# Kernel optimization log

Hardware: AMD Instinct MI355X
Metric: run time of the kernel (lower is better)

The kernel has to match this reference:

```python
import jax, jax.numpy as jnp
import numpy as np

# Cleaned/faithful JAX port of TATLMPLayer. The original torch code has obvious
# typos (edge_type_feature_embedding used before assignment, self.weight_mlp vs
# self._weight_mlp, missing dim= in concatenate, elementwise mult of (B,E,K) with
# (K,D)); we implement the clearly intended math: two-level masked-softmax
# message passing over an incidence matrix H, gumbel-softmax typed edge
# embeddings, and a 4-head cross-attention to polyline features.

NEG_SLOPE = 0.01  # torch leaky_relu default
TAU = 0.5         # gumbel-softmax temperature 1/2


def _mlp(x, W1, b1, W2, b2):
    return jnp.maximum(x @ W1 + b1, 0.0) @ W2 + b2


def setup_inputs() -> dict:
    B, N, E, P, D, T, K, Hd = 2, 256, 512, 256, 128, 8, 8, 256
    key = jax.random.key(0)
    ks = jax.random.split(key, 40)
    g = lambda i, shape, s=0.05: jax.random.normal(ks[i], shape, dtype=jnp.float32) * s
    return {
        "agent_features": jax.random.normal(ks[0], (B, N, D), dtype=jnp.float32),
        "agent_types": jax.random.uniform(ks[1], (B, N, T), dtype=jnp.float32),
        "polyline_features": jax.random.normal(ks[2], (B, P, D), dtype=jnp.float32),
        "H": (jax.random.uniform(ks[3], (B, E, N)) < 0.1).astype(jnp.float32),
        "type_emb": g(4, (K, D)),
        "w_W1": g(5, (2 * D, Hd)), "w_b1": g(6, (Hd,)), "w_W2": g(7, (Hd, 1)), "w_b2": g(8, (1,)),
        "d_W1": g(9, (D + T, Hd)), "d_b1": g(10, (Hd,)), "d_W2": g(11, (Hd, K)), "d_b2": g(12, (K,)),
        "f_W1": g(13, (D + T, Hd)), "f_b1": g(14, (Hd,)), "f_W2": g(15, (Hd, 1)), "f_b2": g(16, (1,)),
        "o_W1": g(17, (4 * D, Hd)), "o_b1": g(18, (Hd,)), "o_W2": g(19, (Hd, D)), "o_b2": g(20, (D,)),
        "q_W": g(21, (3 * D, D)), "q_b": g(22, (D,)),
        "k_W": g(23, (D, D)), "k_b": g(24, (D,)),
        "v_W": g(25, (D, D)), "v_b": g(26, (D,)),
        "iq_W": g(27, (D, D)), "iq_b": g(28, (D,)),
        "ik_W": g(29, (D, D)), "ik_b": g(30, (D,)),
        "iv_W": g(31, (D, D)), "iv_b": g(32, (D,)),
        "op_W": g(33, (D, D)), "op_b": g(34, (D,)),
    }


def reference(agent_features, agent_types, polyline_features, H, type_emb,
              w_W1, w_b1, w_W2, w_b2, d_W1, d_b1, d_W2, d_b2,
              f_W1, f_b1, f_W2, f_b2, o_W1, o_b1, o_W2, o_b2,
              q_W, q_b, k_W, k_b, v_W, v_b,
              iq_W, iq_b, ik_W, ik_b, iv_W, iv_b, op_W, op_b):
    B, N, D = agent_features.shape
    E = H.shape[1]

    # level 1: incidence-aggregated edge features
    ef_init = jnp.einsum('ben,bnd->bed', H, agent_features)            # (B,E,D)
    pair = jnp.concatenate([
        jnp.broadcast_to(ef_init[:, :, None, :], (B, E, N, D)),
        jnp.broadcast_to(agent_features[:, None, :, :], (B, E, N, D))], axis=-1)
    ew = _mlp(pair, w_W1, w_b1, w_W2, w_b2)[..., 0]                    # (B,E,N)
    Hw = jax.nn.softmax(ew * H, axis=2) * H
    edge_features = jnp.einsum('ben,bnd->bed', Hw, agent_features)     # (B,E,D)

    # typed edge embedding via gumbel-softmax over edge types
    edge_type = jnp.einsum('ben,bnt->bet', H, agent_types)             # (B,E,T)
    et = jnp.concatenate([edge_features, edge_type], axis=-1)          # (B,E,D+T)
    logits = _mlp(et, d_W1, d_b1, d_W2, d_b2)                          # (B,E,K)
    u = jax.random.uniform(jax.random.key(42), logits.shape, minval=1e-6, maxval=1.0 - 1e-6)
    gumbel = -jnp.log(-jnp.log(u))
    distribution = jax.nn.softmax((logits + gumbel) / TAU, axis=-1)
    factor = jax.nn.sigmoid(_mlp(et, f_W1, f_b1, f_W2, f_b2))          # (B,E,1)
    edge_type_embedding = jnp.einsum('bek,kd->bed', factor * distribution, type_emb)

    # level 2: masked edge->agent message passing
    pair2 = jnp.concatenate([
        jnp.broadcast_to(edge_type_embedding[:, :, None, :], (B, E, N, D)),
        jnp.broadcast_to(agent_features[:, None, :, :], (B, E, N, D))], axis=-1)
    pair2 = pair2 * H[..., None]
    hw2 = jnp.where(_mlp(pair2, w_W1, w_b1, w_W2, w_b2)[..., 0] > 0,
                    _mlp(pair2, w_W1, w_b1, w_W2, w_b2)[..., 0], 0.0)
    # leaky relu (single-eval form)
    raw2 = _mlp(pair2, w_W1, w_b1, w_W2, w_b2)[..., 0]
    hw2 = jnp.where(raw2 > 0, raw2, NEG_SLOPE * raw2)                  # (B,E,N)
    Hw2 = jax.nn.softmax(hw2, axis=2) * H
    msg = jnp.einsum('ben,bef->bnf', Hw2,
                     jnp.concatenate([edge_features, edge_type_embedding], axis=-1))
    agent_feat = jnp.concatenate([msg, agent_features], axis=-1)       # (B,N,3D)

    # cross-attention to polylines (4 heads)
    Q = agent_feat @ q_W + q_b
    Kp = polyline_features @ k_W + k_b
    Vp = polyline_features @ v_W + v_b
    q2 = Q @ iq_W + iq_b
    k2 = Kp @ ik_W + ik_b
    v2 = Vp @ iv_W + iv_b
    nh, hd = 4, D // 4
    qh = q2.reshape(B, N, nh, hd)
    kh = k2.reshape(B, -1, nh, hd)
    vh = v2.reshape(B, -1, nh, hd)
    att = jax.nn.softmax(jnp.einsum('bqhd,bkhd->bhqk', qh, kh) / jnp.sqrt(jnp.float32(hd)), axis=-1)
    o = jnp.einsum('bhqk,bkhd->bqhd', att, vh).reshape(B, N, D)
    polyline_new = o @ op_W + op_b                                     # (B,N,D)

    agent_new = _mlp(jnp.concatenate([agent_feat, polyline_new], axis=-1),
                     o_W1, o_b1, o_W2, o_b2)                           # (B,N,D)
    return agent_new, polyline_new
```

## Files before the change

### kernel.cpp

```cpp
#include <hip/hip_runtime.h>
#include <math.h>

#define BB 2
#define NN 256
#define EE 512
#define PP 256
#define DD 128
#define TT 8
#define KK 8
#define HDIM 256

#define WS_G      0
#define WS_C0     8192
#define WS_EF0    8256
#define WS_ETYPE  139328
#define WS_V      147520
#define WS_EDGEF  278592
#define WS_ETE    409664
#define WS_HWT    540736
#define WS_AGF    802880
#define WS_Q2     999488
#define WS_K2     1065024
#define WS_V2     1130560

__device__ inline unsigned rotl32(unsigned x, int d){ return (x<<d)|(x>>(32-d)); }

__device__ inline float bits_to_gumbel(unsigned bits){
  float f = __uint_as_float((bits>>9)|0x3f800000u) - 1.0f;
  const float minv = 1e-6f;
  const float maxv = 1.0f - 1e-6f;
  float u = f*(maxv-minv) + minv;
  u = fmaxf(minv, u);
  return -logf(-logf(u));
}

__device__ __forceinline__ void f4fma(float4& a, float x, const float4& w){
  a.x += x*w.x; a.y += x*w.y; a.z += x*w.z; a.w += x*w.w;
}

__device__ __forceinline__ void block_reduce4_max(float v[4], float* wred){
  int lane = threadIdx.x & 63, wid = threadIdx.x >> 6;
  #pragma unroll
  for (int s=32;s>0;s>>=1){
    #pragma unroll
    for (int r=0;r<4;r++){ float o = __shfl_xor(v[r], s, 64); v[r] = fmaxf(v[r],o); }
  }
  if (lane==0){
    #pragma unroll
    for (int r=0;r<4;r++) wred[wid*4+r]=v[r];
  }
  __syncthreads();
  #pragma unroll
  for (int r=0;r<4;r++)
    v[r] = fmaxf(fmaxf(wred[0*4+r],wred[1*4+r]), fmaxf(wred[2*4+r],wred[3*4+r]));
  __syncthreads();
}

__device__ __forceinline__ void block_reduce4_sum(float v[4], float* wred){
  int lane = threadIdx.x & 63, wid = threadIdx.x >> 6;
  #pragma unroll
  for (int s=32;s>0;s>>=1){
    #pragma unroll
    for (int r=0;r<4;r++){ v[r] += __shfl_xor(v[r], s, 64); }
  }
  if (lane==0){
    #pragma unroll
    for (int r=0;r<4;r++) wred[wid*4+r]=v[r];
  }
  __syncthreads();
  #pragma unroll
  for (int r=0;r<4;r++)
    v[r] = (wred[0*4+r]+wred[1*4+r]) + (wred[2*4+r]+wred[3*4+r]);
  __syncthreads();
}

__global__ void prep_kernel(float* g, float* c0, const float* w_b1,
                            const float* w_W2, const float* w_b2,
                            const float* Hm, const float* af, const float* at,
                            float* ef0, float* etype,
                            const float* wW1, float* Vout){
  __shared__ int   ecomp[NN];
  __shared__ int   wcnt[4];
  __shared__ float accl[2][DD];
  __shared__ float acctl[2][TT];
  __shared__ float xs[4][DD];
  __shared__ float part[4*4*HDIM];
  __shared__ float wred[16];
  int blk = blockIdx.x;
  int t = threadIdx.x;
  int lane = t & 63, wid = t >> 6;

  if (blk < 16){
    int j = blk*256 + t;
    {
      const unsigned k0=0u, k1=42u;
      const unsigned ks2 = k0^k1^0x1BD11BDAu;
      unsigned x0 = (unsigned)j, x1 = (unsigned)j + 4096u;
      const int r0[4]={13,15,26,6}, r1[4]={17,29,16,24};
      x0 += k0; x1 += k1;
      #pragma unroll
      for(int i=0;i<4;i++){ x0+=x1; x1=rotl32(x1,r0[i]); x1^=x0; }
      x0+=k1; x1+=ks2+1u;
      #pragma unroll
      for(int i=0;i<4;i++){ x0+=x1; x1=rotl32(x1,r1[i]); x1^=x0; }
      x0+=ks2; x1+=k0+2u;
      #pragma unroll
      for(int i=0;i<4;i++){ x0+=x1; x1=rotl32(x1,r0[i]); x1^=x0; }
      x0+=k0; x1+=k1+3u;
      #pragma unroll
      for(int i=0;i<4;i++){ x0+=x1; x1=rotl32(x1,r1[i]); x1^=x0; }
      x0+=k1; x1+=ks2+4u;
      #pragma unroll
      for(int i=0;i<4;i++){ x0+=x1; x1=rotl32(x1,r0[i]); x1^=x0; }
      x0+=ks2; x1+=k0+5u;
      g[j]      = bits_to_gumbel(x0);
      g[j+4096] = bits_to_gumbel(x1);
    }
    if (blk == 0){
      float v4[4];
      v4[0] = fmaxf(w_b1[t],0.f)*w_W2[t]; v4[1]=0.f; v4[2]=0.f; v4[3]=0.f;
      block_reduce4_sum(v4, wred);
      if (t==0) c0[0] = v4[0] + w_b2[0];
    }
  } else if (blk < 16+BB*EE){
    int be = blk - 16;
    int b  = be / EE;
    const float* Hrow = Hm + (size_t)be*NN;
    int n = t;
    bool pred = (Hrow[n] != 0.f);
    unsigned long long mask = __ballot(pred);
    if (lane==0) wcnt[wid] = __popcll(mask);
    int off = __popcll(mask & ((1ull<<lane)-1ull));
    __syncthreads();
    int wb = 0;
    for (int ww=0; ww<wid; ww++) wb += wcnt[ww];
    if (pred) ecomp[wb+off] = n;
    int total = wcnt[0]+wcnt[1]+wcnt[2]+wcnt[3];
    __syncthreads();
    int d = t & 127, h2 = t >> 7;
    float acc = 0.f, acct = 0.f;
    for (int i=h2; i<total; i+=2){
      int n2 = ecomp[i];
      acc += af[((size_t)b*NN+n2)*DD + d];
      if (d < TT) acct += at[((size_t)b*NN+n2)*TT + d];
    }
    accl[h2][d] = acc;
    if (d < TT) acctl[h2][d] = acct;
    __syncthreads();
    if (t < DD) ef0[(size_t)be*DD + t] = accl[0][t] + accl[1][t];
    if (t < TT) etype[(size_t)be*TT + t] = acctl[0][t] + acctl[1][t];
  } else {
    int r0 = (blk - (16+BB*EE))*4;
    const float* W = wW1 + (size_t)DD*HDIM;
    for (int i=t;i<4*DD;i+=256) xs[i>>7][i&127] = af[(size_t)(r0+(i>>7))*DD + (i&127)];
    __syncthreads();
    int c = (t&63)*4, ks = t>>6;
    float4 acc[4];
    #pragma unroll
    for (int r=0;r<4;r++) acc[r]=make_float4(0.f,0.f,0.f,0.f);
    #pragma unroll 8
    for (int i=ks*32; i<ks*32+32; i++){
      float4 w = *(const float4*)&W[(size_t)i*HDIM + c];
      #pragma unroll
      for (int r=0;r<4;r++) f4fma(acc[r], xs[r][i], w);
    }
    #pragma unroll
    for (int r=0;r<4;r++) *(float4*)&part[(ks*4+r)*HDIM + c] = acc[r];
    __syncthreads();
    #pragma unroll
    for (int r=0;r<4;r++){
      float s = (part[(0*4+r)*HDIM+t] + part[(1*4+r)*HDIM+t])
              + (part[(2*4+r)*HDIM+t] + part[(3*4+r)*HDIM+t]);
      Vout[(size_t)(r0+r)*HDIM + t] = s;
    }
  }
}

__global__ void l1_fused_kernel(const float* ef0, const float* Vm, const float* Hm,
                                const float* af, const float* wW1, const float* wb1,
                                const float* wW2, const float* wb2, float* edgef){
  __shared__ float xs[4][DD];
  __shared__ float part[4*4*HDIM];
  __shared__ float u[4][HDIM];
  __shared__ float w2l[HDIM];
  __shared__ float hwls[4][NN];
  __shared__ float wred[16];
  __shared__ int   ncomp[4][NN];
  __shared__ float ncw[4][NN];
  __shared__ int   ncnt[4];
  int e0 = blockIdx.x*4;
  int b  = e0 >> 9;
  int t  = threadIdx.x;
  int lane = t & 63, wid = t >> 6;

  for (int i=t;i<4*DD;i+=256) xs[i>>7][i&127] = ef0[(size_t)(e0+(i>>7))*DD + (i&127)];
  w2l[t] = wW2[t];
  __syncthreads();
  {
    int c = (t&63)*4, ks = t>>6;
    float4 acc[4];
    #pragma unroll
    for (int r=0;r<4;r++) acc[r]=make_float4(0.f,0.f,0.f,0.f);
    #pragma unroll 8
    for (int i=ks*32; i<ks*32+32; i++){
      float4 w = *(const float4*)&wW1[(size_t)i*HDIM + c];
      #pragma unroll
      for (int r=0;r<4;r++) f4fma(acc[r], xs[r][i], w);
    }
    #pragma unroll
    for (int r=0;r<4;r++) *(float4*)&part[(ks*4+r)*HDIM + c] = acc[r];
  }
  __syncthreads();
  {
    float bv = wb1[t];
    #pragma unroll
    for (int r=0;r<4;r++){
      float s = (part[(0*4+r)*HDIM+t] + part[(1*4+r)*HDIM+t])
              + (part[(2*4+r)*HDIM+t] + part[(3*4+r)*HDIM+t]);
      u[r][t] = s + bv;
    }
  }
  __syncthreads();
  int n = t;
  const float4* Vrow = (const float4*)(Vm + ((size_t)(b*NN)+n)*HDIM);
  float acc[4]={0.f,0.f,0.f,0.f};
  #pragma unroll 4
  for (int ii=0;ii<HDIM/4;ii++){
    float4 v = Vrow[ii];
    float w0=w2l[4*ii+0], w1=w2l[4*ii+1], wc=w2l[4*ii+2], w3=w2l[4*ii+3];
    #pragma unroll
    for (int r=0;r<4;r++){
      acc[r] += fmaxf(u[r][4*ii+0]+v.x,0.f)*w0
              + fmaxf(u[r][4*ii+1]+v.y,0.f)*w1
              + fmaxf(u[r][4*ii+2]+v.z,0.f)*wc
              + fmaxf(u[r][4*ii+3]+v.w,0.f)*w3;
    }
  }
  float b2v = wb2[0];
  float x[4], hv[4];
  #pragma unroll
  for (int r=0;r<4;r++){
    hv[r] = Hm[(size_t)(e0+r)*NN + n];
    x[r] = (hv[r]!=0.f) ? (acc[r]+b2v) : 0.f;
  }
  float m4[4]={x[0],x[1],x[2],x[3]};
  block_reduce4_max(m4, wred);
  float p4[4];
  #pragma unroll
  for (int r=0;r<4;r++) p4[r]=expf(x[r]-m4[r]);
  float s4[4]={p4[0],p4[1],p4[2],p4[3]};
  block_reduce4_sum(s4, wred);
  #pragma unroll
  for (int r=0;r<4;r++)
    hwls[r][n] = (hv[r]!=0.f) ? p4[r]/s4[r] : 0.f;
  __syncthreads();
  {
    int r = wid;
    int base = 0;
    #pragma unroll
    for (int c4=0;c4<4;c4++){
      int n2 = c4*64 + lane;
      float w = hwls[r][n2];
      bool pred = (w != 0.f);
      unsigned long long mask = __ballot(pred);
      int off = __popcll(mask & ((1ull<<lane)-1ull));
      if (pred){ ncomp[r][base+off] = n2; ncw[r][base+off] = w; }
      base += __popcll(mask);
    }
    if (lane==0) ncnt[r] = base;
  }
  __syncthreads();
  {
    int d = t & 127, eh = t >> 7;
    #pragma unroll
    for (int rr=0;rr<2;rr++){
      int r = eh*2 + rr;
      int tot = ncnt[r];
      float a = 0.f;
      for (int i=0;i<tot;i++)
        a += ncw[r][i]*af[((size_t)b*NN+ncomp[r][i])*DD + d];
      edgef[(size_t)(e0+r)*DD + d] = a;
    }
  }
}

__global__ void l2_fused_kernel(const float* edgef, const float* etype, const float* g,
                                const float* dW1, const float* db1, const float* dW2, const float* db2,
                                const float* fW1, const float* fb1, const float* fW2, const float* fb2,
                                const float* type_emb,
                                const float* wW1, const float* wb1, const float* wW2, const float* wb2,
                                const float* c0p, const float* Hm, const float* Vm,
                                float* ete_g, float* HwT){
  __shared__ float et4[4][DD+TT+8];
  __shared__ float part[4*4*HDIM];
  __shared__ float hd4[4][HDIM];
  __shared__ float w2s[HDIM*KK];
  __shared__ float redsm[256];
  __shared__ float wred[16];
  __shared__ float facs[4];
  __shared__ float zz[4][KK];
  __shared__ float pzs[4][KK];
  __shared__ float fdv[4][KK];
  int e0 = blockIdx.x*4;
  int b  = e0 >> 9;
  int t  = threadIdx.x;
  const int KW = DD+TT;

  for (int i=t;i<4*KW;i+=256){
    int r=i/KW, cc=i%KW;
    et4[r][cc] = (cc<DD) ? edgef[(size_t)(e0+r)*DD+cc] : etype[(size_t)(e0+r)*TT + (cc-DD)];
  }
  for (int i=t;i<HDIM*KK;i+=256) w2s[i] = dW2[i];
  __syncthreads();
  int c=(t&63)*4, ks=t>>6;
  {
    float4 a[4];
    #pragma unroll
    for (int r=0;r<4;r++) a[r]=make_float4(0.f,0.f,0.f,0.f);
    #pragma unroll 4
    for (int i=ks*34;i<ks*34+34;i++){
      float4 w = *(const float4*)&dW1[(size_t)i*HDIM+c];
      #pragma unroll
      for (int r=0;r<4;r++) f4fma(a[r], et4[r][i], w);
    }
    #pragma unroll
    for (int r=0;r<4;r++) *(float4*)&part[(ks*4+r)*HDIM+c]=a[r];
  }
  __syncthreads();
  {
    float bd = db1[t];
    #pragma unroll
    for (int r=0;r<4;r++){
      float s = (part[(0*4+r)*HDIM+t]+part[(1*4+r)*HDIM+t])
              + (part[(2*4+r)*HDIM+t]+part[(3*4+r)*HDIM+t]);
      hd4[r][t] = fmaxf(s+bd, 0.f);
    }
  }
  __syncthreads();
  {
    float4 a[4];
    #pragma unroll
    for (int r=0;r<4;r++) a[r]=make_float4(0.f,0.f,0.f,0.f);
    #pragma unroll 4
    for (int i=ks*34;i<ks*34+34;i++){
      float4 w = *(const float4*)&fW1[(size_t)i*HDIM+c];
      #pragma unroll
      for (int r=0;r<4;r++) f4fma(a[r], et4[r][i], w);
    }
    #pragma unroll
    for (int r=0;r<4;r++) *(float4*)&part[(ks*4+r)*HDIM+c]=a[r];
  }
  __syncthreads();
  {
    float bf = fb1[t], fw = fW2[t];
    float v4[4];
    #pragma unroll
    for (int r=0;r<4;r++){
      float s = (part[(0*4+r)*HDIM+t]+part[(1*4+r)*HDIM+t])
              + (part[(2*4+r)*HDIM+t]+part[(3*4+r)*HDIM+t]);
      v4[r] = fmaxf(s+bf,0.f)*fw;
    }
    block_reduce4_sum(v4, wred);
    if (t<4) facs[t] = 1.f/(1.f+expf(-(v4[t]+fb2[0])));
  }
  {
    int rr_ = t>>6, kk_ = (t>>3)&7, jj_ = t&7;
    float lp = 0.f;
    #pragma unroll 4
    for (int h=jj_*32; h<jj_*32+32; h++) lp += hd4[rr_][h]*w2s[h*KK + kk_];
    redsm[t] = lp;
  }
  __syncthreads();
  if (t < 32){
    int r = t>>3, k = t&7;
    float s = db2[k] + g[(size_t)(e0+r)*KK + k];
    #pragma unroll
    for (int j=0;j<8;j++) s += redsm[(r<<6)|(k<<3)|j];
    zz[r][k] = s*2.0f;
  }
  __syncthreads();
  if (t < 32){
    int r = t>>3, k = t&7;
    float m = zz[r][0];
    #pragma unroll
    for (int k2=1;k2<KK;k2++) m = fmaxf(m, zz[r][k2]);
    pzs[r][k] = expf(zz[r][k]-m);
  }
  __syncthreads();
  if (t < 32){
    int r = t>>3, k = t&7;
    float s = 0.f;
    #pragma unroll
    for (int k2=0;k2<KK;k2++) s += pzs[r][k2];
    fdv[r][k] = facs[r]*pzs[r][k]/s;
  }
  __syncthreads();
  {
    int d = t&127;
    #pragma unroll
    for (int rr=0;rr<2;rr++){
      int r = 2*rr + (t>>7);
      float a = 0.f;
      #pragma unroll
      for (int k=0;k<KK;k++) a += fdv[r][k]*type_emb[(size_t)k*DD + d];
      et4[r][d] = a;
      ete_g[(size_t)(e0+r)*DD + d] = a;
    }
    w2s[t] = wW2[t];
  }
  __syncthreads();
  {
    float4 a[4];
    #pragma unroll
    for (int r=0;r<4;r++) a[r]=make_float4(0.f,0.f,0.f,0.f);
    #pragma unroll 8
    for (int i=ks*32;i<ks*32+32;i++){
      float4 w = *(const float4*)&wW1[(size_t)i*HDIM+c];
      #pragma unroll
      for (int r=0;r<4;r++) f4fma(a[r], et4[r][i], w);
    }
    #pragma unroll
    for (int r=0;r<4;r++) *(float4*)&part[(ks*4+r)*HDIM+c]=a[r];
  }
  __syncthreads();
  {
    float bv = wb1[t];
    #pragma unroll
    for (int r=0;r<4;r++){
      float s = (part[(0*4+r)*HDIM+t]+part[(1*4+r)*HDIM+t])
              + (part[(2*4+r)*HDIM+t]+part[(3*4+r)*HDIM+t]);
      hd4[r][t] = s + bv;
    }
  }
  __syncthreads();
  {
    int n = t;
    const float4* Vrow = (const float4*)(Vm + ((size_t)(b*NN)+n)*HDIM);
    float acc[4]={0.f,0.f,0.f,0.f};
    #pragma unroll 4
    for (int ii=0;ii<HDIM/4;ii++){
      float4 v = Vrow[ii];
      float w0=w2s[4*ii+0], w1=w2s[4*ii+1], wc=w2s[4*ii+2], w3=w2s[4*ii+3];
      #pragma unroll
      for (int r=0;r<4;r++){
        acc[r] += fmaxf(hd4[r][4*ii+0]+v.x,0.f)*w0
                + fmaxf(hd4[r][4*ii+1]+v.y,0.f)*w1
                + fmaxf(hd4[r][4*ii+2]+v.z,0.f)*wc
                + fmaxf(hd4[r][4*ii+3]+v.w,0.f)*w3;
      }
    }
    float b2v = wb2[0];
    float c0 = c0p[0];
    float x[4], hv[4];
    #pragma unroll
    for (int r=0;r<4;r++){
      hv[r] = Hm[(size_t)(e0+r)*NN + n];
      float raw = (hv[r]!=0.f) ? (acc[r]+b2v) : c0;
      x[r] = raw>0.f ? raw : 0.01f*raw;
    }
    float m4[4]={x[0],x[1],x[2],x[3]};
    block_reduce4_max(m4, wred);
    float p4[4];
    #pragma unroll
    for (int r=0;r<4;r++) p4[r]=expf(x[r]-m4[r]);
    float s4[4]={p4[0],p4[1],p4[2],p4[3]};
    block_reduce4_sum(s4, wred);
    int eb = e0 & 511;
    float4 o4;
    o4.x = (hv[0]!=0.f)? p4[0]/s4[0] : 0.f;
    o4.y = (hv[1]!=0.f)? p4[1]/s4[1] : 0.f;
    o4.z = (hv[2]!=0.f)? p4[2]/s4[2] : 0.f;
    o4.w = (hv[3]!=0.f)? p4[3]/s4[3] : 0.f;
    *(float4*)(HwT + ((size_t)(b*NN)+n)*EE + eb) = o4;
  }
}

__global__ void msg_kernel(const float* HwT, const float* edgef, const float* ete,
                           const float* af, float* agf){
  __shared__ int   ecomp[EE];
  __shared__ float wcomp[EE];
  __shared__ int wcnt[4];
  int bn = blockIdx.x; int b = bn>>8; int f = threadIdx.x;
  int lane = f & 63, wid = f >> 6;
  const float* wrow = HwT + (size_t)bn*EE;
  int total = 0;
  #pragma unroll
  for (int p=0;p<2;p++){
    int e = p*256 + f;
    float w = wrow[e];
    bool pred = (w != 0.f);
    unsigned long long mask = __ballot(pred);
    if (lane==0) wcnt[wid] = __popcll(mask);
    int off = __popcll(mask & ((1ull<<lane)-1ull));
    __syncthreads();
    int wb = total;
    for (int ww=0; ww<wid; ww++) wb += wcnt[ww];
    if (pred){ ecomp[wb+off] = e; wcomp[wb+off] = w; }
    total += wcnt[0]+wcnt[1]+wcnt[2]+wcnt[3];
    __syncthreads();
  }
  float acc = 0.f;
  const float* srcbase = (f < DD) ? (edgef + (size_t)b*EE*DD + f)
                                  : (ete   + (size_t)b*EE*DD + (f-DD));
  for (int i=0;i<total;i++){
    acc += wcomp[i] * srcbase[(size_t)ecomp[i]*DD];
  }
  agf[(size_t)bn*(3*DD)+f] = acc;
  if (f < DD) agf[(size_t)bn*(3*DD) + 2*DD + f] = af[(size_t)bn*DD + f];
}

__device__ __forceinline__ void mlp128_lds(const float (*in)[DD], const float* W, const float* bias,
                                           float (*outl)[DD], float* part, int t){
  int c=(t&31)*4, ks=t>>5;
  float4 a[4];
  #pragma unroll
  for (int r=0;r<4;r++) a[r]=make_float4(0.f,0.f,0.f,0.f);
  #pragma unroll 4
  for (int i=ks*16;i<ks*16+16;i++){
    float4 w = *(const float4*)&W[(size_t)i*DD+c];
    #pragma unroll
    for (int r=0;r<4;r++) f4fma(a[r], in[r][i], w);
  }
  #pragma unroll
  for (int r=0;r<4;r++) *(float4*)&part[(ks*4+r)*DD+c]=a[r];
  __syncthreads();
  int cc=t&127, rh=t>>7;
  for (int rr=rh; rr<4; rr+=2){
    float s=0.f;
    #pragma unroll
    for (int k2=0;k2<8;k2++) s+=part[(k2*4+rr)*DD+cc];
    outl[rr][cc]=s+bias[cc];
  }
  __syncthreads();
}

__device__ __forceinline__ void mlp128_glob(const float (*in)[DD], const float* W, const float* bias,
                                            float* dst, int r0, float* part, int t){
  int c=(t&31)*4, ks=t>>5;
  float4 a[4];
  #pragma unroll
  for (int r=0;r<4;r++) a[r]=make_float4(0.f,0.f,0.f,0.f);
  #pragma unroll 4
  for (int i=ks*16;i<ks*16+16;i++){
    float4 w = *(const float4*)&W[(size_t)i*DD+c];
    #pragma unroll
    for (int r=0;r<4;r++) f4fma(a[r], in[r][i], w);
  }
  #pragma unroll
  for (int r=0;r<4;r++) *(float4*)&part[(ks*4+r)*DD+c]=a[r];
  __syncthreads();
  int cc=t&127, rh=t>>7;
  for (int rr=rh; rr<4; rr+=2){
    float s=0.f;
    #pragma unroll
    for (int k2=0;k2<8;k2++) s+=part[(k2*4+rr)*DD+cc];
    dst[(size_t)(r0+rr)*DD+cc]=s+bias[cc];
  }
  __syncthreads();
}

__global__ void q2kv_kernel(const float* agf, const float* qW, const float* qb,
                            const float* iqW, const float* iqb,
                            const float* pf,
                            const float* kW, const float* kb, const float* ikW, const float* ikb,
                            const float* vW, const float* vb, const float* ivW, const float* ivb,
                            float* q2, float* k2, float* v2){
  __shared__ float xs[4][3*DD];
  __shared__ float bufA[4][DD];
  __shared__ float bufB[4][DD];
  __shared__ float part[8*4*DD];
  int t = threadIdx.x;
  if (blockIdx.x < 128){
    int r0 = blockIdx.x*4;
    #pragma unroll
    for (int r=0;r<4;r++)
      for (int cc=t;cc<3*DD;cc+=256) xs[r][cc] = agf[(size_t)(r0+r)*(3*DD)+cc];
    __syncthreads();
    int c=(t&31)*4, ks=t>>5;
    float4 a[4];
    #pragma unroll
    for (int r=0;r<4;r++) a[r]=make_float4(0.f,0.f,0.f,0.f);
    #pragma unroll 4
    for (int i=ks*48;i<ks*48+48;i++){
      float4 w = *(const float4*)&qW[(size_t)i*DD+c];
      #pragma unroll
      for (int r=0;r<4;r++) f4fma(a[r], xs[r][i], w);
    }
    #pragma unroll
    for (int r=0;r<4;r++) *(float4*)&part[(ks*4+r)*DD+c]=a[r];
    __syncthreads();
    int cc=t&127, rh=t>>7;
    for (int rr=rh; rr<4; rr+=2){
      float s=0.f;
      #pragma unroll
      for (int k2_=0;k2_<8;k2_++) s+=part[(k2_*4+rr)*DD+cc];
      bufA[rr][cc]=s+qb[cc];
    }
    __syncthreads();
    mlp128_glob(bufA, iqW, iqb, q2, r0, part, t);
  } else {
    int r0 = (blockIdx.x-128)*4;
    for (int i=t;i<4*DD;i+=256) bufA[i>>7][i&127] = pf[(size_t)(r0+(i>>7))*DD + (i&127)];
    __syncthreads();
    mlp128_lds (bufA, kW, kb, bufB, part, t);
    mlp128_glob(bufB, ikW, ikb, k2, r0, part, t);
    mlp128_lds (bufA, vW, vb, bufB, part, t);
    mlp128_glob(bufB, ivW, ivb, v2, r0, part, t);
  }
}

__global__ void attn2_kernel(const float* q2, const float* k2, const float* v2,
                             const float* op_W, const float* op_b, float* pnew){
  __shared__ float qr[2][DD];
  __shared__ float att[2][4][PP+1];
  __shared__ float o_l[2][DD];
  __shared__ float part[8*2*DD];
  int r0 = blockIdx.x*2; int b = r0 >> 8; int t = threadIdx.x;
  for (int i=t;i<2*DD;i+=256) qr[i>>7][i&127] = q2[(size_t)(r0+(i>>7))*DD + (i&127)];
  __syncthreads();
  const float scale = 0.17677669529663687f;
  const float* krow = k2 + ((size_t)(b*PP) + t)*DD;
  #pragma unroll
  for (int h=0;h<4;h++){
    const float4* k4 = (const float4*)(krow + h*32);
    float s[2]={0.f,0.f};
    #pragma unroll
    for (int jj=0;jj<8;jj++){
      float4 kk = k4[jj];
      #pragma unroll
      for (int r=0;r<2;r++){
        s[r] += qr[r][h*32+jj*4+0]*kk.x + qr[r][h*32+jj*4+1]*kk.y
              + qr[r][h*32+jj*4+2]*kk.z + qr[r][h*32+jj*4+3]*kk.w;
      }
    }
    #pragma unroll
    for (int r=0;r<2;r++) att[r][h][t] = s[r]*scale;
  }
  __syncthreads();
  {
    int lane = t & 63, wid = t >> 6;
    for (int q = wid; q < 8; q += 4){
      int r = q >> 2, h = q & 3;
      float v0 = att[r][h][lane],     v1 = att[r][h][lane+64],
            ve = att[r][h][lane+128], v3 = att[r][h][lane+192];
      float m = fmaxf(fmaxf(v0,v1), fmaxf(ve,v3));
      #pragma unroll
      for (int s2=32;s2>0;s2>>=1) m = fmaxf(m, __shfl_xor(m, s2, 64));
      float e0 = expf(v0-m), e1 = expf(v1-m), e2 = expf(ve-m), e3 = expf(v3-m);
      float ss = (e0+e1)+(e2+e3);
      #pragma unroll
      for (int s2=32;s2>0;s2>>=1) ss += __shfl_xor(ss, s2, 64);
      float inv = 1.f/ss;
      att[r][h][lane] = e0*inv; att[r][h][lane+64] = e1*inv;
      att[r][h][lane+128] = e2*inv; att[r][h][lane+192] = e3*inv;
    }
  }
  __syncthreads();
  int c=(t&31)*4, ps=t>>5; int h2 = c>>5;
  {
    float4 acc[2];
    #pragma unroll
    for (int r=0;r<2;r++) acc[r]=make_float4(0.f,0.f,0.f,0.f);
    #pragma unroll 4
    for (int i=0;i<32;i++){
      int p = ps*32+i;
      float4 v = *(const float4*)&v2[((size_t)(b*PP)+p)*DD + c];
      #pragma unroll
      for (int r=0;r<2;r++) f4fma(acc[r], att[r][h2][p], v);
    }
    #pragma unroll
    for (int r=0;r<2;r++) *(float4*)&part[(ps*2+r)*DD+c]=acc[r];
  }
  __syncthreads();
  {
    int cc=t&127, r=t>>7;
    float s=0.f;
    #pragma unroll
    for (int k2_=0;k2_<8;k2_++) s+=part[(k2_*2+r)*DD+cc];
    o_l[r][cc]=s;
  }
  __syncthreads();
  {
    float4 a2[2];
    #pragma unroll
    for (int r=0;r<2;r++) a2[r]=make_float4(0.f,0.f,0.f,0.f);
    #pragma unroll 4
    for (int i=ps*16;i<ps*16+16;i++){
      float4 w = *(const float4*)&op_W[(size_t)i*DD + c];
      #pragma unroll
      for (int r=0;r<2;r++) f4fma(a2[r], o_l[r][i], w);
    }
    #pragma unroll
    for (int r=0;r<2;r++) *(float4*)&part[(ps*2+r)*DD+c]=a2[r];
  }
  __syncthreads();
  {
    int cc=t&127, r=t>>7;
    float s=0.f;
    #pragma unroll
    for (int k2_=0;k2_<8;k2_++) s+=part[(k2_*2+r)*DD+cc];
    pnew[(size_t)(r0+r)*DD+cc]=s+op_b[cc];
  }
}

__global__ void final2_kernel(const float* agf, const float* pnewv,
                              const float* oW1, const float* ob1,
                              const float* oW2, const float* ob2, float* anew){
  __shared__ float xs[2][4*DD];
  __shared__ float hid[2][HDIM];
  __shared__ float part[4*2*HDIM];
  int r0 = blockIdx.x*2; int t = threadIdx.x;
  for (int i=t;i<2*(4*DD);i+=256){
    int r = i>>9, cc = i&511;
    xs[r][cc] = (cc<3*DD) ? agf[(size_t)(r0+r)*(3*DD)+cc]
                          : pnewv[(size_t)(r0+r)*DD + (cc-3*DD)];
  }
  __syncthreads();
  {
    int c=(t&63)*4, ks=t>>6;
    float4 acc[2];
    #pragma unroll
    for (int r=0;r<2;r++) acc[r]=make_float4(0.f,0.f,0.f,0.f);
    #pragma unroll 8
    for (int i=ks*128;i<ks*128+128;i++){
      float4 w = *(const float4*)&oW1[(size_t)i*HDIM+c];
      #pragma unroll
      for (int r=0;r<2;r++) f4fma(acc[r], xs[r][i], w);
    }
    #pragma unroll
    for (int r=0;r<2;r++) *(float4*)&part[(ks*2+r)*HDIM+c]=acc[r];
  }
  __syncthreads();
  {
    float bv = ob1[t];
    #pragma unroll
    for (int r=0;r<2;r++){
      float s = (part[(0*2+r)*HDIM+t]+part[(1*2+r)*HDIM+t])
              + (part[(2*2+r)*HDIM+t]+part[(3*2+r)*HDIM+t]);
      hid[r][t] = fmaxf(s+bv, 0.f);
    }
  }
  __syncthreads();
  {
    int c2=(t&31)*4, ks2=t>>5;
    float4 a2[2];
    #pragma unroll
    for (int r=0;r<2;r++) a2[r]=make_float4(0.f,0.f,0.f,0.f);
    #pragma unroll 8
    for (int h=ks2*32;h<ks2*32+32;h++){
      float4 w = *(const float4*)&oW2[(size_t)h*DD+c2];
      #pragma unroll
      for (int r=0;r<2;r++) f4fma(a2[r], hid[r][h], w);
    }
    #pragma unroll
    for (int r=0;r<2;r++) *(float4*)&part[(ks2*2+r)*DD+c2]=a2[r];
  }
  __syncthreads();
  {
    int cc=t&127, r=t>>7;
    float s=0.f;
    #pragma unroll
    for (int k2_=0;k2_<8;k2_++) s+=part[(k2_*2+r)*DD+cc];
    anew[(size_t)(r0+r)*DD+cc]=s+ob2[cc];
  }
}

extern "C" void kernel_launch(void* const* d_in, const int* in_sizes, int n_in,
                              void* d_out, int out_size, void* d_ws, size_t ws_size,
                              hipStream_t stream) {
  const float* af       = (const float*)d_in[0];
  const float* at       = (const float*)d_in[1];
  const float* pf       = (const float*)d_in[2];
  const float* Hm       = (const float*)d_in[3];
  const float* type_emb = (const float*)d_in[4];
  const float* w_W1 = (const float*)d_in[5];
  const float* w_b1 = (const float*)d_in[6];
  const float* w_W2 = (const float*)d_in[7];
  const float* w_b2 = (const float*)d_in[8];
  const float* d_W1 = (const float*)d_in[9];
  const float* d_b1 = (const float*)d_in[10];
  const float* d_W2 = (const float*)d_in[11];
  const float* d_b2 = (const float*)d_in[12];
  const float* f_W1 = (const float*)d_in[13];
  const float* f_b1 = (const float*)d_in[14];
  const float* f_W2 = (const float*)d_in[15];
  const float* f_b2 = (const float*)d_in[16];
  const float* o_W1 = (const float*)d_in[17];
  const float* o_b1 = (const float*)d_in[18];
  const float* o_W2 = (const float*)d_in[19];
  const float* o_b2 = (const float*)d_in[20];
  const float* q_W  = (const float*)d_in[21];
  const float* q_b  = (const float*)d_in[22];
  const float* k_W  = (const float*)d_in[23];
  const float* k_b  = (const float*)d_in[24];
  const float* v_W  = (const float*)d_in[25];
  const float* v_b  = (const float*)d_in[26];
  const float* iq_W = (const float*)d_in[27];
  const float* iq_b = (const float*)d_in[28];
  const float* ik_W = (const float*)d_in[29];
  const float* ik_b = (const float*)d_in[30];
  const float* iv_W = (const float*)d_in[31];
  const float* iv_b = (const float*)d_in[32];
  const float* op_W = (const float*)d_in[33];
  const float* op_b = (const float*)d_in[34];

  float* ws   = (float*)d_ws;
  float* out  = (float*)d_out;
  float* anew = out;
  float* pnew = out + BB*NN*DD;

  prep_kernel<<<16+BB*EE+128, 256, 0, stream>>>(
      ws+WS_G, ws+WS_C0, w_b1, w_W2, w_b2,
      Hm, af, at, ws+WS_EF0, ws+WS_ETYPE, w_W1, ws+WS_V);
  l1_fused_kernel<<<256,256,0,stream>>>(
      ws+WS_EF0, ws+WS_V, Hm, af, w_W1, w_b1, w_W2, w_b2, ws+WS_EDGEF);
  l2_fused_kernel<<<256,256,0,stream>>>(
      ws+WS_EDGEF, ws+WS_ETYPE, ws+WS_G,
      d_W1,d_b1,d_W2,d_b2, f_W1,f_b1,f_W2,f_b2, type_emb,
      w_W1, w_b1, w_W2, w_b2, ws+WS_C0, Hm, ws+WS_V,
      ws+WS_ETE, ws+WS_HWT);
  msg_kernel<<<BB*NN,256,0,stream>>>(ws+WS_HWT, ws+WS_EDGEF, ws+WS_ETE, af, ws+WS_AGF);
  q2kv_kernel<<<256,256,0,stream>>>(ws+WS_AGF, q_W,q_b,iq_W,iq_b, pf,
                                    k_W,k_b,ik_W,ik_b, v_W,v_b,iv_W,iv_b,
                                    ws+WS_Q2, ws+WS_K2, ws+WS_V2);
  attn2_kernel<<<256,256,0,stream>>>(ws+WS_Q2, ws+WS_K2, ws+WS_V2, op_W, op_b, pnew);
  final2_kernel<<<256,256,0,stream>>>(ws+WS_AGF, pnew, o_W1,o_b1,o_W2,o_b2, anew);
}
```

Measured before the change: 104.4 us.

## Fuse Q projection into msg kernel, attention into final MLP, K/V into prep

```diff
diff --git a/kernel.cpp b/kernel.cpp
--- a/kernel.cpp
+++ b/kernel.cpp
@@ -23,6 +23,11 @@
 #define WS_K2     1065024
 #define WS_V2     1130560
 
+#define GB_INC  16
+#define GB_V    1040
+#define GB_KV   1168
+#define GB_END  1296
+
 __device__ inline unsigned rotl32(unsigned x, int d){ return (x<<d)|(x>>(32-d)); }
 
 __device__ inline float bits_to_gumbel(unsigned bits){
@@ -74,11 +79,65 @@
   __syncthreads();
 }
 
+__device__ __forceinline__ void mlp128_lds(const float (*in)[DD], const float* W, const float* bias,
+                                           float (*outl)[DD], float* part, int t){
+  int c=(t&31)*4, ks=t>>5;
+  float4 a[4];
+  #pragma unroll
+  for (int r=0;r<4;r++) a[r]=make_float4(0.f,0.f,0.f,0.f);
+  #pragma unroll 4
+  for (int i=ks*16;i<ks*16+16;i++){
+    float4 w = *(const float4*)&W[(size_t)i*DD+c];
+    #pragma unroll
+    for (int r=0;r<4;r++) f4fma(a[r], in[r][i], w);
+  }
+  #pragma unroll
+  for (int r=0;r<4;r++) *(float4*)&part[(ks*4+r)*DD+c]=a[r];
+  __syncthreads();
+  int cc=t&127, rh=t>>7;
+  for (int rr=rh; rr<4; rr+=2){
+    float s=0.f;
+    #pragma unroll
+    for (int k2=0;k2<8;k2++) s+=part[(k2*4+rr)*DD+cc];
+    outl[rr][cc]=s+bias[cc];
+  }
+  __syncthreads();
+}
+
+__device__ __forceinline__ void mlp128_glob(const float (*in)[DD], const float* W, const float* bias,
+                                            float* dst, int r0, float* part, int t){
+  int c=(t&31)*4, ks=t>>5;
+  float4 a[4];
+  #pragma unroll
+  for (int r=0;r<4;r++) a[r]=make_float4(0.f,0.f,0.f,0.f);
+  #pragma unroll 4
+  for (int i=ks*16;i<ks*16+16;i++){
+    float4 w = *(const float4*)&W[(size_t)i*DD+c];
+    #pragma unroll
+    for (int r=0;r<4;r++) f4fma(a[r], in[r][i], w);
+  }
+  #pragma unroll
+  for (int r=0;r<4;r++) *(float4*)&part[(ks*4+r)*DD+c]=a[r];
+  __syncthreads();
+  int cc=t&127, rh=t>>7;
+  for (int rr=rh; rr<4; rr+=2){
+    float s=0.f;
+    #pragma unroll
+    for (int k2=0;k2<8;k2++) s+=part[(k2*4+rr)*DD+cc];
+    dst[(size_t)(r0+rr)*DD+cc]=s+bias[cc];
+  }
+  __syncthreads();
+}
+
 __global__ void prep_kernel(float* g, float* c0, const float* w_b1,
                             const float* w_W2, const float* w_b2,
                             const float* Hm, const float* af, const float* at,
                             float* ef0, float* etype,
-                            const float* wW1, float* Vout){
+                            const float* wW1, float* Vout,
+                            const float* pf,
+                            const float* kW, const float* kb, const float* ikW, const float* ikb,
+                            const float* vW, const float* vb, const float* ivW, const float* ivb,
+                            float* k2, float* v2){
   __shared__ int   ecomp[NN];
   __shared__ int   wcnt[4];
   __shared__ float accl[2][DD];
@@ -86,11 +145,12 @@
   __shared__ float xs[4][DD];
   __shared__ float part[4*4*HDIM];
   __shared__ float wred[16];
+  __shared__ float bufB[4][DD];
   int blk = blockIdx.x;
   int t = threadIdx.x;
   int lane = t & 63, wid = t >> 6;
 
-  if (blk < 16){
+  if (blk < GB_INC){
     int j = blk*256 + t;
     {
       const unsigned k0=0u, k1=42u;
@@ -122,9 +182,9 @@
       block_reduce4_sum(v4, wred);
       if (t==0) c0[0] = v4[0] + w_b2[0];
     }
-  } else if (blk < 16+BB*EE){
-    int be = blk - 16;
-    int b  = be / EE;
+  } else if (blk < GB_V){
+    int be = blk - GB_INC;
+    int b  = be >> 9;
     const float* Hrow = Hm + (size_t)be*NN;
     int n = t;
     bool pred = (Hrow[n] != 0.f);
@@ -149,8 +209,8 @@
     __syncthreads();
     if (t < DD) ef0[(size_t)be*DD + t] = accl[0][t] + accl[1][t];
     if (t < TT) etype[(size_t)be*TT + t] = acctl[0][t] + acctl[1][t];
-  } else {
-    int r0 = (blk - (16+BB*EE))*4;
+  } else if (blk < GB_KV){
+    int r0 = (blk - GB_V)*4;
     const float* W = wW1 + (size_t)DD*HDIM;
     for (int i=t;i<4*DD;i+=256) xs[i>>7][i&127] = af[(size_t)(r0+(i>>7))*DD + (i&127)];
     __syncthreads();
@@ -173,6 +233,14 @@
               + (part[(2*4+r)*HDIM+t] + part[(3*4+r)*HDIM+t]);
       Vout[(size_t)(r0+r)*HDIM + t] = s;
     }
+  } else {
+    int r0 = (blk - GB_KV)*4;
+    for (int i=t;i<4*DD;i+=256) xs[i>>7][i&127] = pf[(size_t)(r0+(i>>7))*DD + (i&127)];
+    __syncthreads();
+    mlp128_lds (xs, kW, kb, bufB, part, t);
+    mlp128_glob(bufB, ikW, ikb, k2, r0, part, t);
+    mlp128_lds (xs, vW, vb, bufB, part, t);
+    mlp128_glob(bufB, ivW, ivb, v2, r0, part, t);
   }
 }
 
@@ -292,7 +360,8 @@
                                 const float* c0p, const float* Hm, const float* Vm,
                                 float* ete_g, float* HwT){
   __shared__ float et4[4][DD+TT+8];
-  __shared__ float part[4*4*HDIM];
+  __shared__ float partD[4*4*HDIM];
+  __shared__ float partF[4*4*HDIM];
   __shared__ float hd4[4][HDIM];
   __shared__ float w2s[HDIM*KK];
   __shared__ float redsm[256];
@@ -314,51 +383,35 @@
   __syncthreads();
   int c=(t&63)*4, ks=t>>6;
   {
-    float4 a[4];
-    #pragma unroll
-    for (int r=0;r<4;r++) a[r]=make_float4(0.f,0.f,0.f,0.f);
+    float4 ad4[4], af4[4];
+    #pragma unroll
+    for (int r=0;r<4;r++){ ad4[r]=make_float4(0.f,0.f,0.f,0.f); af4[r]=make_float4(0.f,0.f,0.f,0.f); }
     #pragma unroll 4
     for (int i=ks*34;i<ks*34+34;i++){
-      float4 w = *(const float4*)&dW1[(size_t)i*HDIM+c];
-      #pragma unroll
-      for (int r=0;r<4;r++) f4fma(a[r], et4[r][i], w);
-    }
-    #pragma unroll
-    for (int r=0;r<4;r++) *(float4*)&part[(ks*4+r)*HDIM+c]=a[r];
+      float4 wd = *(const float4*)&dW1[(size_t)i*HDIM+c];
+      float4 wf = *(const float4*)&fW1[(size_t)i*HDIM+c];
+      #pragma unroll
+      for (int r=0;r<4;r++){ float x=et4[r][i]; f4fma(ad4[r],x,wd); f4fma(af4[r],x,wf); }
+    }
+    #pragma unroll
+    for (int r=0;r<4;r++){
+      *(float4*)&partD[(ks*4+r)*HDIM+c]=ad4[r];
+      *(float4*)&partF[(ks*4+r)*HDIM+c]=af4[r];
+    }
   }
   __syncthreads();
   {
     float bd = db1[t];
-    #pragma unroll
-    for (int r=0;r<4;r++){
-      float s = (part[(0*4+r)*HDIM+t]+part[(1*4+r)*HDIM+t])
-              + (part[(2*4+r)*HDIM+t]+part[(3*4+r)*HDIM+t]);
-      hd4[r][t] = fmaxf(s+bd, 0.f);
-    }
-  }
-  __syncthreads();
-  {
-    float4 a[4];
-    #pragma unroll
-    for (int r=0;r<4;r++) a[r]=make_float4(0.f,0.f,0.f,0.f);
-    #pragma unroll 4
-    for (int i=ks*34;i<ks*34+34;i++){
-      float4 w = *(const float4*)&fW1[(size_t)i*HDIM+c];
-      #pragma unroll
-      for (int r=0;r<4;r++) f4fma(a[r], et4[r][i], w);
-    }
-    #pragma unroll
-    for (int r=0;r<4;r++) *(float4*)&part[(ks*4+r)*HDIM+c]=a[r];
-  }
-  __syncthreads();
-  {
     float bf = fb1[t], fw = fW2[t];
     float v4[4];
     #pragma unroll
     for (int r=0;r<4;r++){
-      float s = (part[(0*4+r)*HDIM+t]+part[(1*4+r)*HDIM+t])
-              + (part[(2*4+r)*HDIM+t]+part[(3*4+r)*HDIM+t]);
-      v4[r] = fmaxf(s+bf,0.f)*fw;
+      float sd = (partD[(0*4+r)*HDIM+t]+partD[(1*4+r)*HDIM+t])
+               + (partD[(2*4+r)*HDIM+t]+partD[(3*4+r)*HDIM+t]);
+      hd4[r][t] = fmaxf(sd+bd, 0.f);
+      float sf = (partF[(0*4+r)*HDIM+t]+partF[(1*4+r)*HDIM+t])
+               + (partF[(2*4+r)*HDIM+t]+partF[(3*4+r)*HDIM+t]);
+      v4[r] = fmaxf(sf+bf,0.f)*fw;
     }
     block_reduce4_sum(v4, wred);
     if (t<4) facs[t] = 1.f/(1.f+expf(-(v4[t]+fb2[0])));
@@ -367,7 +420,10 @@
     int rr_ = t>>6, kk_ = (t>>3)&7, jj_ = t&7;
     float lp = 0.f;
     #pragma unroll 4
-    for (int h=jj_*32; h<jj_*32+32; h++) lp += hd4[rr_][h]*w2s[h*KK + kk_];
+    for (int i=0;i<32;i++){
+      int h = jj_ + 8*i;
+      lp += hd4[rr_][h]*w2s[h*KK + kk_];
+    }
     redsm[t] = lp;
   }
   __syncthreads();
@@ -420,15 +476,15 @@
       for (int r=0;r<4;r++) f4fma(a[r], et4[r][i], w);
     }
     #pragma unroll
-    for (int r=0;r<4;r++) *(float4*)&part[(ks*4+r)*HDIM+c]=a[r];
+    for (int r=0;r<4;r++) *(float4*)&partD[(ks*4+r)*HDIM+c]=a[r];
   }
   __syncthreads();
   {
     float bv = wb1[t];
     #pragma unroll
     for (int r=0;r<4;r++){
-      float s = (part[(0*4+r)*HDIM+t]+part[(1*4+r)*HDIM+t])
-              + (part[(2*4+r)*HDIM+t]+part[(3*4+r)*HDIM+t]);
+      float s = (partD[(0*4+r)*HDIM+t]+partD[(1*4+r)*HDIM+t])
+              + (partD[(2*4+r)*HDIM+t]+partD[(3*4+r)*HDIM+t]);
       hd4[r][t] = s + bv;
     }
   }
@@ -475,11 +531,16 @@
   }
 }
 
-__global__ void msg_kernel(const float* HwT, const float* edgef, const float* ete,
-                           const float* af, float* agf){
+__global__ void msgq2_kernel(const float* HwT, const float* edgef, const float* ete,
+                             const float* af, const float* qW, const float* qb,
+                             const float* iqW, const float* iqb,
+                             float* agf, float* q2){
   __shared__ int   ecomp[EE];
   __shared__ float wcomp[EE];
-  __shared__ int wcnt[4];
+  __shared__ int   wcnt[4];
+  __shared__ float agfl[3*DD];
+  __shared__ float part[8*DD];
+  __shared__ float Qs[DD];
   int bn = blockIdx.x; int b = bn>>8; int f = threadIdx.x;
   int lane = f & 63, wid = f >> 6;
   const float* wrow = HwT + (size_t)bn*EE;
@@ -505,116 +566,63 @@
   for (int i=0;i<total;i++){
     acc += wcomp[i] * srcbase[(size_t)ecomp[i]*DD];
   }
+  agfl[f] = acc;
   agf[(size_t)bn*(3*DD)+f] = acc;
-  if (f < DD) agf[(size_t)bn*(3*DD) + 2*DD + f] = af[(size_t)bn*DD + f];
-}
-
-__device__ __forceinline__ void mlp128_lds(const float (*in)[DD], const float* W, const float* bias,
-                                           float (*outl)[DD], float* part, int t){
-  int c=(t&31)*4, ks=t>>5;
-  float4 a[4];
-  #pragma unroll
-  for (int r=0;r<4;r++) a[r]=make_float4(0.f,0.f,0.f,0.f);
-  #pragma unroll 4
-  for (int i=ks*16;i<ks*16+16;i++){
-    float4 w = *(const float4*)&W[(size_t)i*DD+c];
-    #pragma unroll
-    for (int r=0;r<4;r++) f4fma(a[r], in[r][i], w);
-  }
-  #pragma unroll
-  for (int r=0;r<4;r++) *(float4*)&part[(ks*4+r)*DD+c]=a[r];
-  __syncthreads();
-  int cc=t&127, rh=t>>7;
-  for (int rr=rh; rr<4; rr+=2){
-    float s=0.f;
-    #pragma unroll
-    for (int k2=0;k2<8;k2++) s+=part[(k2*4+rr)*DD+cc];
-    outl[rr][cc]=s+bias[cc];
-  }
-  __syncthreads();
-}
-
-__device__ __forceinline__ void mlp128_glob(const float (*in)[DD], const float* W, const float* bias,
-                                            float* dst, int r0, float* part, int t){
-  int c=(t&31)*4, ks=t>>5;
-  float4 a[4];
-  #pragma unroll
-  for (int r=0;r<4;r++) a[r]=make_float4(0.f,0.f,0.f,0.f);
-  #pragma unroll 4
-  for (int i=ks*16;i<ks*16+16;i++){
-    float4 w = *(const float4*)&W[(size_t)i*DD+c];
-    #pragma unroll
-    for (int r=0;r<4;r++) f4fma(a[r], in[r][i], w);
-  }
-  #pragma unroll
-  for (int r=0;r<4;r++) *(float4*)&part[(ks*4+r)*DD+c]=a[r];
-  __syncthreads();
-  int cc=t&127, rh=t>>7;
-  for (int rr=rh; rr<4; rr+=2){
-    float s=0.f;
-    #pragma unroll
-    for (int k2=0;k2<8;k2++) s+=part[(k2*4+rr)*DD+cc];
-    dst[(size_t)(r0+rr)*DD+cc]=s+bias[cc];
-  }
-  __syncthreads();
-}
-
-__global__ void q2kv_kernel(const float* agf, const float* qW, const float* qb,
-                            const float* iqW, const float* iqb,
-                            const float* pf,
-                            const float* kW, const float* kb, const float* ikW, const float* ikb,
-                            const float* vW, const float* vb, const float* ivW, const float* ivb,
-                            float* q2, float* k2, float* v2){
-  __shared__ float xs[4][3*DD];
-  __shared__ float bufA[4][DD];
-  __shared__ float bufB[4][DD];
-  __shared__ float part[8*4*DD];
-  int t = threadIdx.x;
-  if (blockIdx.x < 128){
-    int r0 = blockIdx.x*4;
-    #pragma unroll
-    for (int r=0;r<4;r++)
-      for (int cc=t;cc<3*DD;cc+=256) xs[r][cc] = agf[(size_t)(r0+r)*(3*DD)+cc];
-    __syncthreads();
-    int c=(t&31)*4, ks=t>>5;
-    float4 a[4];
-    #pragma unroll
-    for (int r=0;r<4;r++) a[r]=make_float4(0.f,0.f,0.f,0.f);
+  if (f < DD){
+    float av = af[(size_t)bn*DD + f];
+    agfl[2*DD+f] = av;
+    agf[(size_t)bn*(3*DD) + 2*DD + f] = av;
+  }
+  __syncthreads();
+  int c=(f&31)*4, ks=f>>5;
+  {
+    float4 a = make_float4(0.f,0.f,0.f,0.f);
     #pragma unroll 4
     for (int i=ks*48;i<ks*48+48;i++){
       float4 w = *(const float4*)&qW[(size_t)i*DD+c];
-      #pragma unroll
-      for (int r=0;r<4;r++) f4fma(a[r], xs[r][i], w);
-    }
-    #pragma unroll
-    for (int r=0;r<4;r++) *(float4*)&part[(ks*4+r)*DD+c]=a[r];
-    __syncthreads();
-    int cc=t&127, rh=t>>7;
-    for (int rr=rh; rr<4; rr+=2){
-      float s=0.f;
-      #pragma unroll
-      for (int k2_=0;k2_<8;k2_++) s+=part[(k2_*4+rr)*DD+cc];
-      bufA[rr][cc]=s+qb[cc];
-    }
-    __syncthreads();
-    mlp128_glob(bufA, iqW, iqb, q2, r0, part, t);
-  } else {
-    int r0 = (blockIdx.x-128)*4;
-    for (int i=t;i<4*DD;i+=256) bufA[i>>7][i&127] = pf[(size_t)(r0+(i>>7))*DD + (i&127)];
-    __syncthreads();
-    mlp128_lds (bufA, kW, kb, bufB, part, t);
-    mlp128_glob(bufB, ikW, ikb, k2, r0, part, t);
-    mlp128_lds (bufA, vW, vb, bufB, part, t);
-    mlp128_glob(bufB, ivW, ivb, v2, r0, part, t);
-  }
-}
-
-__global__ void attn2_kernel(const float* q2, const float* k2, const float* v2,
-                             const float* op_W, const float* op_b, float* pnew){
+      f4fma(a, agfl[i], w);
+    }
+    *(float4*)&part[ks*DD+c]=a;
+  }
+  __syncthreads();
+  if (f<DD){
+    float s=0.f;
+    #pragma unroll
+    for (int k=0;k<8;k++) s+=part[k*DD+f];
+    Qs[f]=s+qb[f];
+  }
+  __syncthreads();
+  {
+    float4 a = make_float4(0.f,0.f,0.f,0.f);
+    #pragma unroll 4
+    for (int i=ks*16;i<ks*16+16;i++){
+      float4 w = *(const float4*)&iqW[(size_t)i*DD+c];
+      f4fma(a, Qs[i], w);
+    }
+    *(float4*)&part[ks*DD+c]=a;
+  }
+  __syncthreads();
+  if (f<DD){
+    float s=0.f;
+    #pragma unroll
+    for (int k=0;k<8;k++) s+=part[k*DD+f];
+    q2[(size_t)bn*DD+f]=s+iqb[f];
+  }
+}
+
+__global__ void attnfinal_kernel(const float* q2, const float* k2, const float* v2,
+                                 const float* op_W, const float* op_b,
+                                 const float* agf,
+                                 const float* oW1, const float* ob1,
+                                 const float* oW2, const float* ob2,
+                                 float* pnew, float* anew){
   __shared__ float qr[2][DD];
   __shared__ float att[2][4][PP+1];
   __shared__ float o_l[2][DD];
   __shared__ float part[8*2*DD];
+  __shared__ float pnl[2][DD];
+  __shared__ float xs[2][4*DD];
+  __shared__ float hid[2][HDIM];
   int r0 = blockIdx.x*2; int b = r0 >> 8; int t = threadIdx.x;
   for (int i=t;i<2*DD;i+=256) qr[i>>7][i&127] = q2[(size_t)(r0+(i>>7))*DD + (i&127)];
   __syncthreads();
@@ -699,36 +707,33 @@
     float s=0.f;
     #pragma unroll
     for (int k2_=0;k2_<8;k2_++) s+=part[(k2_*2+r)*DD+cc];
-    pnew[(size_t)(r0+r)*DD+cc]=s+op_b[cc];
-  }
-}
-
-__global__ void final2_kernel(const float* agf, const float* pnewv,
-                              const float* oW1, const float* ob1,
-                              const float* oW2, const float* ob2, float* anew){
-  __shared__ float xs[2][4*DD];
-  __shared__ float hid[2][HDIM];
-  __shared__ float part[4*2*HDIM];
-  int r0 = blockIdx.x*2; int t = threadIdx.x;
-  for (int i=t;i<2*(4*DD);i+=256){
-    int r = i>>9, cc = i&511;
-    xs[r][cc] = (cc<3*DD) ? agf[(size_t)(r0+r)*(3*DD)+cc]
-                          : pnewv[(size_t)(r0+r)*DD + (cc-3*DD)];
-  }
-  __syncthreads();
-  {
-    int c=(t&63)*4, ks=t>>6;
+    float pv = s+op_b[cc];
+    pnl[r][cc] = pv;
+    pnew[(size_t)(r0+r)*DD+cc] = pv;
+  }
+  for (int i=t;i<2*(3*DD);i+=256){
+    int r = i/(3*DD), cc = i%(3*DD);
+    xs[r][cc] = agf[(size_t)(r0+r)*(3*DD)+cc];
+  }
+  __syncthreads();
+  if (t < 2*DD){
+    int r = t>>7, cc = t&127;
+    xs[r][3*DD+cc] = pnl[r][cc];
+  }
+  __syncthreads();
+  {
+    int c1=(t&63)*4, ks1=t>>6;
     float4 acc[2];
     #pragma unroll
     for (int r=0;r<2;r++) acc[r]=make_float4(0.f,0.f,0.f,0.f);
     #pragma unroll 8
-    for (int i=ks*128;i<ks*128+128;i++){
-      float4 w = *(const float4*)&oW1[(size_t)i*HDIM+c];
+    for (int i=ks1*128;i<ks1*128+128;i++){
+      float4 w = *(const float4*)&oW1[(size_t)i*HDIM+c1];
       #pragma unroll
       for (int r=0;r<2;r++) f4fma(acc[r], xs[r][i], w);
     }
     #pragma unroll
-    for (int r=0;r<2;r++) *(float4*)&part[(ks*2+r)*HDIM+c]=acc[r];
+    for (int r=0;r<2;r++) *(float4*)&part[(ks1*2+r)*HDIM+c1]=acc[r];
   }
   __syncthreads();
   {
@@ -742,18 +747,17 @@
   }
   __syncthreads();
   {
-    int c2=(t&31)*4, ks2=t>>5;
     float4 a2[2];
     #pragma unroll
     for (int r=0;r<2;r++) a2[r]=make_float4(0.f,0.f,0.f,0.f);
     #pragma unroll 8
-    for (int h=ks2*32;h<ks2*32+32;h++){
-      float4 w = *(const float4*)&oW2[(size_t)h*DD+c2];
+    for (int h=ps*32;h<ps*32+32;h++){
+      float4 w = *(const float4*)&oW2[(size_t)h*DD+c];
       #pragma unroll
       for (int r=0;r<2;r++) f4fma(a2[r], hid[r][h], w);
     }
     #pragma unroll
-    for (int r=0;r<2;r++) *(float4*)&part[(ks2*2+r)*DD+c2]=a2[r];
+    for (int r=0;r<2;r++) *(float4*)&part[(ps*2+r)*DD+c]=a2[r];
   }
   __syncthreads();
   {
@@ -809,9 +813,11 @@
   float* anew = out;
   float* pnew = out + BB*NN*DD;
 
-  prep_kernel<<<16+BB*EE+128, 256, 0, stream>>>(
+  prep_kernel<<<GB_END, 256, 0, stream>>>(
       ws+WS_G, ws+WS_C0, w_b1, w_W2, w_b2,
-      Hm, af, at, ws+WS_EF0, ws+WS_ETYPE, w_W1, ws+WS_V);
+      Hm, af, at, ws+WS_EF0, ws+WS_ETYPE, w_W1, ws+WS_V,
+      pf, k_W,k_b,ik_W,ik_b, v_W,v_b,iv_W,iv_b,
+      ws+WS_K2, ws+WS_V2);
   l1_fused_kernel<<<256,256,0,stream>>>(
       ws+WS_EF0, ws+WS_V, Hm, af, w_W1, w_b1, w_W2, w_b2, ws+WS_EDGEF);
   l2_fused_kernel<<<256,256,0,stream>>>(
@@ -819,10 +825,10 @@
       d_W1,d_b1,d_W2,d_b2, f_W1,f_b1,f_W2,f_b2, type_emb,
       w_W1, w_b1, w_W2, w_b2, ws+WS_C0, Hm, ws+WS_V,
       ws+WS_ETE, ws+WS_HWT);
-  msg_kernel<<<BB*NN,256,0,stream>>>(ws+WS_HWT, ws+WS_EDGEF, ws+WS_ETE, af, ws+WS_AGF);
-  q2kv_kernel<<<256,256,0,stream>>>(ws+WS_AGF, q_W,q_b,iq_W,iq_b, pf,
-                                    k_W,k_b,ik_W,ik_b, v_W,v_b,iv_W,iv_b,
-                                    ws+WS_Q2, ws+WS_K2, ws+WS_V2);
-  attn2_kernel<<<256,256,0,stream>>>(ws+WS_Q2, ws+WS_K2, ws+WS_V2, op_W, op_b, pnew);
-  final2_kernel<<<256,256,0,stream>>>(ws+WS_AGF, pnew, o_W1,o_b1,o_W2,o_b2, anew);
-}
+  msgq2_kernel<<<BB*NN,256,0,stream>>>(
+      ws+WS_HWT, ws+WS_EDGEF, ws+WS_ETE, af,
+      q_W, q_b, iq_W, iq_b, ws+WS_AGF, ws+WS_Q2);
+  attnfinal_kernel<<<256,256,0,stream>>>(
+      ws+WS_Q2, ws+WS_K2, ws+WS_V2, op_W, op_b,
+      ws+WS_AGF, o_W1,o_b1,o_W2,o_b2, pnew, anew);
+}
```

Measured after the change: 91.78 us. 12.1% less time.
